# Performance work log

Hardware: AMD Instinct MI355X
Metric: run time of the kernel (lower is better)

The kernel has to match this reference:

```python
import jax, jax.numpy as jnp
import numpy as np

B, S, D = 8, 2048, 512
E, DF = 16, 2048  # total experts, FFN hidden (4*d_model)
K = 4             # num_available_experts


def setup_inputs() -> dict:
    key = jax.random.key(0)
    ks = jax.random.split(key, 5)
    scale = 0.02
    return {
        "x": jax.random.normal(ks[0], (B, S, D), dtype=jnp.float32),
        "gate_w": jax.random.normal(ks[1], (E, D), dtype=jnp.float32) * scale,
        "gate_b": jnp.zeros((E,), dtype=jnp.float32),
        "w1": jax.random.normal(ks[2], (E, D, DF), dtype=jnp.float32) * scale,
        "b1": jnp.zeros((E, DF), dtype=jnp.float32),
        "w2": jax.random.normal(ks[3], (E, DF, D), dtype=jnp.float32) * scale,
        "b2": jnp.zeros((E, D), dtype=jnp.float32),
        "num_available": K,
    }


def reference(x, gate_w, gate_b, w1, b1, w2, b2, num_available):
    # Coarse expert selection: gate applied to the global token sum k = sum_{b,s} x
    k = jnp.sum(x, axis=(0, 1))                       # [D]
    coarse = gate_w @ k + gate_b                      # [E]
    _, idx = jax.lax.top_k(coarse, num_available)     # [K]

    # Gather selected experts' params
    gw_w, gw_b = gate_w[idx], gate_b[idx]             # [K,D], [K]
    W1, B1 = w1[idx], b1[idx]                         # [K,D,DF], [K,DF]
    W2, B2 = w2[idx], b2[idx]                         # [K,DF,D], [K,D]

    # Per-token softmax gating over the K selected experts
    logits = jnp.einsum('bsd,kd->bsk', x, gw_w) + gw_b  # [B,S,K]
    gw = jax.nn.softmax(logits, axis=2)                 # [B,S,K]

    # Dense expert FFNs over all tokens, weighted combine
    h = jax.nn.gelu(jnp.einsum('bsd,kdf->kbsf', x, W1) + B1[:, None, None, :])  # [K,B,S,DF]
    eo = jnp.einsum('kbsf,kfd->kbsd', h, W2) + B2[:, None, None, :]             # [K,B,S,D]
    out = jnp.einsum('kbsd,bsk->bsd', eo, gw)                                   # [B,S,D]
    return out
```

## Files before the change

### kernel.cpp

```cpp
#include <hip/hip_runtime.h>
#include <hip/hip_bf16.h>
#include <cstdint>
#include <cstddef>

typedef __attribute__((ext_vector_type(8))) short short8;
typedef __attribute__((ext_vector_type(4))) float f32x4;

#define AS1U32(p) ((const __attribute__((address_space(1))) uint32_t*)(p))
#define AS3U32(p) ((__attribute__((address_space(3))) uint32_t*)(p))

__device__ __forceinline__ unsigned short f2bf(float v) {
  union { float f; uint32_t u; } a; a.f = v;
  uint32_t u = a.u;
  u += 0x7FFFu + ((u >> 16) & 1u);
  return (unsigned short)(u >> 16);
}

__device__ __forceinline__ float gelu_fast(float x) {
  const float A = -2.302118142f;
  const float B = -0.102943494f;
  float x2 = x * x;
  float t = x * __builtin_fmaf(B, x2, A);
  float e = __builtin_amdgcn_exp2f(t);
  return x * __builtin_amdgcn_rcpf(1.0f + e);
}


__global__ __launch_bounds__(512)
void reduce_part(const float* __restrict__ x, float* __restrict__ kpart) {
  const int d = threadIdx.x;
  const int b = blockIdx.x;
  float s = 0.f;
#pragma unroll 4
  for (int i = 0; i < 64; i++)
    s += x[((size_t)b * 64 + i) * 512 + d];
  kpart[(size_t)b * 512 + d] = s;
}

__global__ __launch_bounds__(1024)
void gate_all(const float* __restrict__ kpart,
              const float* __restrict__ gate_w,
              const float* __restrict__ gate_b,
              const float* __restrict__ b1, const float* __restrict__ b2,
              int* __restrict__ idxout,
              float* __restrict__ b1cat, float* __restrict__ b2sel) {
  __shared__ float ksum2[2][512];
  __shared__ float coarse[16];
  __shared__ int idxl[4];
  const int t = threadIdx.x;
  {
    const int d = t & 511, h = t >> 9;
    float s = 0.f;
    for (int p = h * 128; p < h * 128 + 128; p++) s += kpart[(size_t)p * 512 + d];
    ksum2[h][d] = s;
  }
  __syncthreads();
  {
    const int wave = t >> 6, lane = t & 63;
    const int d0 = lane * 8;
    float s = 0.f;
#pragma unroll
    for (int j = 0; j < 8; j++)
      s += gate_w[wave * 512 + d0 + j] * (ksum2[0][d0 + j] + ksum2[1][d0 + j]);
#pragma unroll
    for (int off = 32; off >= 1; off >>= 1) s += __shfl_down(s, off, 64);
    if (lane == 0) coarse[wave] = s + gate_b[wave];
  }
  __syncthreads();
  if (t == 0) {
    unsigned taken = 0;
    for (int r = 0; r < 4; r++) {
      float best = -3.4e38f; int bi = 0;
      for (int e = 0; e < 16; e++)
        if (!((taken >> e) & 1u) && coarse[e] > best) { best = coarse[e]; bi = e; }
      taken |= 1u << bi;
      idxl[r] = bi; idxout[r] = bi;
    }
  }
  __syncthreads();
  for (int i = t; i < 8192; i += 1024)
    b1cat[i] = b1[(size_t)idxl[i >> 11] * 2048 + (i & 2047)];
  for (int i = t; i < 2048; i += 1024)
    b2sel[i] = b2[(size_t)idxl[i >> 9] * 512 + (i & 511)];
}

__global__ __launch_bounds__(256)
void transpose_all(const float* __restrict__ w1, const float* __restrict__ w2,
                   unsigned short* __restrict__ w1t, unsigned short* __restrict__ w2t,
                   const int* __restrict__ idx) {
  __shared__ float tl[64][65];
  const int tid = threadIdx.x;
  const int ty = tid >> 6, tx = tid & 63;
  const int z = blockIdx.z;
  const float* src; unsigned short* dbase; int C, dstLd, r0, c0;
  if (z < 4) {
    src = w1 + (size_t)idx[z] * 512 * 2048;
    dbase = w1t + (size_t)z * 2048 * 512;
    C = 2048; dstLd = 512;
    r0 = blockIdx.x * 64; c0 = blockIdx.y * 64;
  } else {
    src = w2 + (size_t)idx[z - 4] * 2048 * 512;
    dbase = w2t + (size_t)(z - 4) * 2048;
    C = 512; dstLd = 8192;
    r0 = blockIdx.y * 64; c0 = blockIdx.x * 64;
  }
#pragma unroll
  for (int i = 0; i < 16; i++) {
    int r = ty * 16 + i;
    tl[r][tx] = src[(size_t)(r0 + r) * C + c0 + tx];
  }
  __syncthreads();
#pragma unroll
  for (int i = 0; i < 16; i++) {
    int rr = ty * 16 + i;
    dbase[(size_t)(c0 + rr) * dstLd + r0 + tx] = f2bf(tl[tx][rr]);
  }
}

__global__ __launch_bounds__(256)
void gate_softmax_xconv(const float* __restrict__ x,
                        const float* __restrict__ gate_w,
                        const float* __restrict__ gate_b,
                        const int* __restrict__ idx,
                        float* __restrict__ gwout,
                        unsigned short* __restrict__ xbf) {
  __shared__ float wsel[4][512];
  __shared__ float bsel[4];
  const int tid = threadIdx.x;
  for (int i = tid; i < 2048; i += 256) {
    int k = i >> 9;
    wsel[k][i & 511] = gate_w[(size_t)idx[k] * 512 + (i & 511)];
  }
  if (tid < 4) bsel[tid] = gate_b[idx[tid]];
  __syncthreads();
  const int wave = tid >> 6, lane = tid & 63;
  const int t = blockIdx.x * 4 + wave;
  const float* xr = x + (size_t)t * 512 + lane * 8;
  float4 v0 = ((const float4*)xr)[0];
  float4 v1 = ((const float4*)xr)[1];
  float vals[8] = {v0.x, v0.y, v0.z, v0.w, v1.x, v1.y, v1.z, v1.w};
  short8 pk;
#pragma unroll
  for (int j = 0; j < 8; j++) pk[j] = (short)f2bf(vals[j]);
  *(short8*)(xbf + (size_t)t * 512 + lane * 8) = pk;
  float a0 = 0.f, a1 = 0.f, a2 = 0.f, a3 = 0.f;
  const int dbase = lane * 8;
#pragma unroll
  for (int j = 0; j < 8; j++) {
    float xv = vals[j];
    a0 += xv * wsel[0][dbase + j];
    a1 += xv * wsel[1][dbase + j];
    a2 += xv * wsel[2][dbase + j];
    a3 += xv * wsel[3][dbase + j];
  }
#pragma unroll
  for (int off = 32; off >= 1; off >>= 1) {
    a0 += __shfl_down(a0, off, 64);
    a1 += __shfl_down(a1, off, 64);
    a2 += __shfl_down(a2, off, 64);
    a3 += __shfl_down(a3, off, 64);
  }
  if (lane == 0) {
    float l0 = a0 + bsel[0], l1 = a1 + bsel[1], l2 = a2 + bsel[2], l3 = a3 + bsel[3];
    float m = fmaxf(fmaxf(l0, l1), fmaxf(l2, l3));
    float e0 = __expf(l0 - m), e1 = __expf(l1 - m);
    float e2 = __expf(l2 - m), e3 = __expf(l3 - m);
    float inv = 1.0f / (e0 + e1 + e2 + e3);
    float* o = gwout + (size_t)t * 4;
    o[0] = e0 * inv; o[1] = e1 * inv; o[2] = e2 * inv; o[3] = e3 * inv;
  }
}


#define CFENCE asm volatile("" ::: "memory")
#define BAR    do { CFENCE; __builtin_amdgcn_s_barrier(); CFENCE; } while (0)
#define LGKM0  do { asm volatile("s_waitcnt lgkmcnt(0)" ::: "memory"); \
                    __builtin_amdgcn_sched_barrier(0); } while (0)
#define SCHEDB __builtin_amdgcn_sched_barrier(0)
#define VMW(n) asm volatile("s_waitcnt vmcnt(" #n ")" ::: "memory")

#define LDALL(abuf, bbuf)                                                   \
  do {                                                                      \
    _Pragma("unroll")                                                       \
    for (int i_ = 0; i_ < 4; i_++)                                          \
      _Pragma("unroll")                                                     \
      for (int ks_ = 0; ks_ < 2; ks_++)                                     \
        aF[i_][ks_] = *(const short8*)((abuf) +                             \
            (size_t)(wm + i_ * 16 + fr) * 64 +                              \
            (((ks_ * 4 + quad) ^ swz) << 3));                               \
    _Pragma("unroll")                                                       \
    for (int j_ = 0; j_ < 4; j_++)                                          \
      _Pragma("unroll")                                                     \
      for (int ks_ = 0; ks_ < 2; ks_++)                                     \
        bF[j_][ks_] = *(const short8*)((bbuf) +                             \
            (size_t)(wn + j_ * 16 + fr) * 64 +                              \
            (((ks_ * 4 + quad) ^ swz) << 3));                               \
  } while (0)

#define MMH(ks)                                                             \
  do {                                                                      \
    __builtin_amdgcn_s_setprio(1);                                          \
    _Pragma("unroll")                                                       \
    for (int i_ = 0; i_ < 4; i_++)                                          \
      _Pragma("unroll")                                                     \
      for (int j_ = 0; j_ < 4; j_++)                                        \
        acc[i_][j_] = __builtin_amdgcn_mfma_f32_16x16x32_bf16(              \
            aF[i_][ks], bF[j_][ks], acc[i_][j_], 0, 0, 0);                  \
    __builtin_amdgcn_s_setprio(0);                                          \
  } while (0)

template <int EPI>
__global__ __launch_bounds__(256, 2)
void gemm4p(const unsigned short* __restrict__ A,
            const unsigned short* __restrict__ Bt,
            void* __restrict__ C, int K, int lda, int ldb, int ldc,
            const float* __restrict__ gw,
            const float* __restrict__ bias, int colOff, int accum) {
  __shared__ unsigned short lds[4 * 128 * 64];
  const int tid = threadIdx.x;
  const int wave = tid >> 6, lane = tid & 63;
  const int lrow = lane >> 3, lslot = lane & 7, gch = lslot ^ lrow;
  const int fr = lane & 15, quad = lane >> 4, swz = fr & 7;
  const int wm = (wave >> 1) * 64, wn = (wave & 1) * 64;
  const int rowA0 = blockIdx.x * 128;
  const int rowB0 = blockIdx.y * 128;

  unsigned short* const A0 = lds;
  unsigned short* const B0 = lds + 128 * 64;
  unsigned short* const A1 = lds + 2 * 128 * 64;
  unsigned short* const B1 = lds + 3 * 128 * 64;

  auto stT = [&](unsigned short* ab, unsigned short* bb, int kt) {
#pragma unroll
    for (int c = 0; c < 4; c++) {
      int r = wave * 32 + c * 8 + lrow;
      const unsigned short* gp = A + (size_t)(rowA0 + r) * lda + kt + gch * 8;
      __builtin_amdgcn_global_load_lds(AS1U32(gp), AS3U32(ab + (wave * 32 + c * 8) * 64), 16, 0, 0);
    }
#pragma unroll
    for (int c = 0; c < 4; c++) {
      int r = wave * 32 + c * 8 + lrow;
      const unsigned short* gp = Bt + (size_t)(rowB0 + r) * ldb + kt + gch * 8;
      __builtin_amdgcn_global_load_lds(AS1U32(gp), AS3U32(bb + (wave * 32 + c * 8) * 64), 16, 0, 0);
    }
  };

  f32x4 acc[4][4];
#pragma unroll
  for (int i = 0; i < 4; i++)
#pragma unroll
    for (int j = 0; j < 4; j++) acc[i][j] = (f32x4){0.f, 0.f, 0.f, 0.f};

  short8 aF[4][2];
  short8 bF[4][2];

  stT(A0, B0, 0);
  stT(A1, B1, 64);
  VMW(8);
  BAR;

  const int niter = K >> 7;
  for (int i = 0; i < niter - 1; i++) {
    const int kt = i * 128;
    LDALL(A0, B0);
    BAR; LGKM0; MMH(0); BAR;
    stT(A0, B0, kt + 128); SCHEDB;
    MMH(1); VMW(8); BAR;
    LDALL(A1, B1);
    BAR; LGKM0; MMH(0); BAR;
    stT(A1, B1, kt + 192); SCHEDB;
    MMH(1); VMW(8); BAR;
  }
  LDALL(A0, B0);
  BAR; LGKM0; MMH(0); BAR;
  MMH(1); VMW(0); BAR;
  LDALL(A1, B1);
  BAR; LGKM0; MMH(0); BAR;
  MMH(1);

  if (EPI == 1) {
    unsigned short* Cb = (unsigned short*)C;
    const int kexp = (colOff + rowB0) >> 11;
#pragma unroll
    for (int i = 0; i < 4; i++) {
#pragma unroll
      for (int reg = 0; reg < 4; reg++) {
        int r = rowA0 + wm + i * 16 + quad * 4 + reg;
        float g = gw[(size_t)r * 4 + kexp];
#pragma unroll
        for (int j = 0; j < 4; j++) {
          int n = rowB0 + wn + j * 16 + fr;
          float v = acc[i][j][reg] + bias[colOff + n];
          Cb[(size_t)r * ldc + n] = f2bf(gelu_fast(v) * g);
        }
      }
    }
  } else {
    float* Cf = (float*)C;
#pragma unroll
    for (int i = 0; i < 4; i++) {
#pragma unroll
      for (int reg = 0; reg < 4; reg++) {
        int r = rowA0 + wm + i * 16 + quad * 4 + reg;
        size_t t4 = (size_t)r * 4;
        float g0 = gw[t4], g1 = gw[t4 + 1], g2 = gw[t4 + 2], g3 = gw[t4 + 3];
#pragma unroll
        for (int j = 0; j < 4; j++) {
          int n = rowB0 + wn + j * 16 + fr;
          size_t ci = (size_t)r * 512 + n;
          float v = acc[i][j][reg];
          if (accum) v += Cf[ci];
          else v += g0 * bias[n] + g1 * bias[512 + n] +
                    g2 * bias[1024 + n] + g3 * bias[1536 + n];
          Cf[ci] = v;
        }
      }
    }
  }
}

#undef LDALL
#undef MMH


extern "C" void kernel_launch(void* const* d_in, const int* in_sizes, int n_in,
                              void* d_out, int out_size, void* d_ws, size_t ws_size,
                              hipStream_t stream) {
  (void)in_sizes; (void)n_in; (void)out_size;
  const float* x      = (const float*)d_in[0];
  const float* gate_w = (const float*)d_in[1];
  const float* gate_b = (const float*)d_in[2];
  const float* w1     = (const float*)d_in[3];
  const float* b1     = (const float*)d_in[4];
  const float* w2     = (const float*)d_in[5];
  const float* b2     = (const float*)d_in[6];

  char* ws = (char*)d_ws;
  int*            idx   = (int*)(ws + 0);
  float*          gw    = (float*)(ws + 4096);
  float*          b1cat = (float*)(ws + 266240);
  float*          b2sel = (float*)(ws + 299008);
  float*          kpart = (float*)(ws + 307200);
  unsigned short* xbf   = (unsigned short*)(ws + 831488);
  unsigned short* w1t   = (unsigned short*)(ws + 17608704);
  unsigned short* w2t   = (unsigned short*)(ws + 25997312);
  unsigned short* hbuf  = (unsigned short*)(ws + 34385920);
  const size_t HBUF_OFF = 34385920;

  size_t avail = ws_size > HBUF_OFF ? ws_size - HBUF_OFF : 0;
  int nslab = 1;
  while (nslab < 16 && (size_t)16384 * (8192 / nslab) * 2 > avail) nslab <<= 1;
  const int slabDF = 8192 / nslab;

  reduce_part<<<256, 512, 0, stream>>>(x, kpart);
  gate_all<<<1, 1024, 0, stream>>>(kpart, gate_w, gate_b, b1, b2, idx, b1cat, b2sel);
  transpose_all<<<dim3(8, 32, 8), 256, 0, stream>>>(w1, w2, w1t, w2t, idx);
  gate_softmax_xconv<<<4096, 256, 0, stream>>>(x, gate_w, gate_b, idx, gw, xbf);

  for (int s = 0; s < nslab; s++) {
    const int c0 = s * slabDF;
    gemm4p<1><<<dim3(128, slabDF / 128), 256, 0, stream>>>(
        xbf, w1t + (size_t)c0 * 512, hbuf,
        512, 512, 512, slabDF,
        gw, b1cat, c0, 0);
    gemm4p<2><<<dim3(128, 4), 256, 0, stream>>>(
        hbuf, w2t + c0, (float*)d_out,
        slabDF, slabDF, 8192, 512,
        gw, b2sel, 0, s > 0);
  }
}
```

Before: 502.1 us.

## Fuse prep kernels, vectorize transpose, and add simpler direct-to-LDS GEMM for first FFN

Merges the weight transpose and the gate-softmax/bf16-conversion kernels into one launch. The transpose now moves float4/ushort4 vectors per thread. The first FFN GEMM is replaced by a new single-buffered GEMM that loads global memory straight into swizzled LDS and runs bf16 MFMA 16x16x32 with two blocks per CU. The token-sum reduction also uses fewer, longer partial sums. This cuts launch overhead and narrow memory accesses, but the new GEMM drops the software pipelining of the old gemm4p and may hide memory latency less well.

```diff
diff --git a/kernel.cpp b/kernel.cpp
--- a/kernel.cpp
+++ b/kernel.cpp
@@ -32,8 +32,8 @@
   const int b = blockIdx.x;
   float s = 0.f;
 #pragma unroll 4
-  for (int i = 0; i < 64; i++)
-    s += x[((size_t)b * 64 + i) * 512 + d];
+  for (int i = 0; i < 128; i++)
+    s += x[((size_t)b * 128 + i) * 512 + d];
   kpart[(size_t)b * 512 + d] = s;
 }
 
@@ -51,7 +51,7 @@
   {
     const int d = t & 511, h = t >> 9;
     float s = 0.f;
-    for (int p = h * 128; p < h * 128 + 128; p++) s += kpart[(size_t)p * 512 + d];
+    for (int p = h * 64; p < h * 64 + 64; p++) s += kpart[(size_t)p * 512 + d];
     ksum2[h][d] = s;
   }
   __syncthreads();
@@ -85,89 +85,206 @@
 }
 
 __global__ __launch_bounds__(256)
-void transpose_all(const float* __restrict__ w1, const float* __restrict__ w2,
-                   unsigned short* __restrict__ w1t, unsigned short* __restrict__ w2t,
-                   const int* __restrict__ idx) {
-  __shared__ float tl[64][65];
+void prep_fused(const float* __restrict__ x,
+                const float* __restrict__ gate_w,
+                const float* __restrict__ gate_b,
+                const int* __restrict__ idx,
+                float* __restrict__ gwout,
+                unsigned short* __restrict__ xbf,
+                const float* __restrict__ w1, const float* __restrict__ w2,
+                unsigned short* __restrict__ w1t, unsigned short* __restrict__ w2t) {
+  __shared__ float smem[64 * 65];
   const int tid = threadIdx.x;
-  const int ty = tid >> 6, tx = tid & 63;
-  const int z = blockIdx.z;
-  const float* src; unsigned short* dbase; int C, dstLd, r0, c0;
-  if (z < 4) {
-    src = w1 + (size_t)idx[z] * 512 * 2048;
-    dbase = w1t + (size_t)z * 2048 * 512;
-    C = 2048; dstLd = 512;
-    r0 = blockIdx.x * 64; c0 = blockIdx.y * 64;
+  const int bid = blockIdx.x;
+
+  if (bid < 4096) {
+    float* wsel = smem;
+    float* bsel = smem + 2048;
+    for (int i = tid; i < 2048; i += 256) {
+      int k = i >> 9;
+      wsel[(size_t)k * 512 + (i & 511)] = gate_w[(size_t)idx[k] * 512 + (i & 511)];
+    }
+    if (tid < 4) bsel[tid] = gate_b[idx[tid]];
+    __syncthreads();
+    const int wave = tid >> 6, lane = tid & 63;
+    const int t = bid * 4 + wave;
+    const float* xr = x + (size_t)t * 512 + lane * 8;
+    float4 v0 = ((const float4*)xr)[0];
+    float4 v1 = ((const float4*)xr)[1];
+    float vals[8] = {v0.x, v0.y, v0.z, v0.w, v1.x, v1.y, v1.z, v1.w};
+    short8 pk;
+#pragma unroll
+    for (int j = 0; j < 8; j++) pk[j] = (short)f2bf(vals[j]);
+    *(short8*)(xbf + (size_t)t * 512 + lane * 8) = pk;
+    float a0 = 0.f, a1 = 0.f, a2 = 0.f, a3 = 0.f;
+    const int dbase = lane * 8;
+#pragma unroll
+    for (int j = 0; j < 8; j++) {
+      float xv = vals[j];
+      a0 += xv * wsel[dbase + j];
+      a1 += xv * wsel[512 + dbase + j];
+      a2 += xv * wsel[1024 + dbase + j];
+      a3 += xv * wsel[1536 + dbase + j];
+    }
+#pragma unroll
+    for (int off = 32; off >= 1; off >>= 1) {
+      a0 += __shfl_down(a0, off, 64);
+      a1 += __shfl_down(a1, off, 64);
+      a2 += __shfl_down(a2, off, 64);
+      a3 += __shfl_down(a3, off, 64);
+    }
+    if (lane == 0) {
+      float l0 = a0 + bsel[0], l1 = a1 + bsel[1], l2 = a2 + bsel[2], l3 = a3 + bsel[3];
+      float m = fmaxf(fmaxf(l0, l1), fmaxf(l2, l3));
+      float e0 = __expf(l0 - m), e1 = __expf(l1 - m);
+      float e2 = __expf(l2 - m), e3 = __expf(l3 - m);
+      float inv = 1.0f / (e0 + e1 + e2 + e3);
+      float* o = gwout + (size_t)t * 4;
+      o[0] = e0 * inv; o[1] = e1 * inv; o[2] = e2 * inv; o[3] = e3 * inv;
+    }
   } else {
-    src = w2 + (size_t)idx[z - 4] * 2048 * 512;
-    dbase = w2t + (size_t)(z - 4) * 2048;
-    C = 512; dstLd = 8192;
-    r0 = blockIdx.y * 64; c0 = blockIdx.x * 64;
-  }
-#pragma unroll
-  for (int i = 0; i < 16; i++) {
-    int r = ty * 16 + i;
-    tl[r][tx] = src[(size_t)(r0 + r) * C + c0 + tx];
-  }
-  __syncthreads();
-#pragma unroll
-  for (int i = 0; i < 16; i++) {
-    int rr = ty * 16 + i;
-    dbase[(size_t)(c0 + rr) * dstLd + r0 + tx] = f2bf(tl[tx][rr]);
-  }
-}
-
-__global__ __launch_bounds__(256)
-void gate_softmax_xconv(const float* __restrict__ x,
-                        const float* __restrict__ gate_w,
-                        const float* __restrict__ gate_b,
-                        const int* __restrict__ idx,
-                        float* __restrict__ gwout,
-                        unsigned short* __restrict__ xbf) {
-  __shared__ float wsel[4][512];
-  __shared__ float bsel[4];
+    const int zz = bid - 4096;
+    const int z = zz >> 8;
+    const int rem = zz & 255;
+    const int bx = rem & 7, by = rem >> 3;
+    const float* src; unsigned short* dbase; int C, dstLd, r0, c0;
+    if (z < 4) {
+      src = w1 + (size_t)idx[z] * 512 * 2048;
+      dbase = w1t + (size_t)z * 2048 * 512;
+      C = 2048; dstLd = 512;
+      r0 = bx * 64; c0 = by * 64;
+    } else {
+      src = w2 + (size_t)idx[z - 4] * 2048 * 512;
+      dbase = w2t + (size_t)(z - 4) * 2048;
+      C = 512; dstLd = 8192;
+      r0 = by * 64; c0 = bx * 64;
+    }
+    float (*tl)[65] = (float(*)[65])smem;
+    const int tx4 = (tid & 15) * 4;
+    const int ty = tid >> 4;
+#pragma unroll
+    for (int i = 0; i < 4; i++) {
+      int r = i * 16 + ty;
+      float4 v = *(const float4*)&src[(size_t)(r0 + r) * C + c0 + tx4];
+      tl[r][tx4 + 0] = v.x; tl[r][tx4 + 1] = v.y;
+      tl[r][tx4 + 2] = v.z; tl[r][tx4 + 3] = v.w;
+    }
+    __syncthreads();
+#pragma unroll
+    for (int i = 0; i < 4; i++) {
+      int rr = i * 16 + ty;
+      ushort4 o;
+      o.x = f2bf(tl[tx4 + 0][rr]);
+      o.y = f2bf(tl[tx4 + 1][rr]);
+      o.z = f2bf(tl[tx4 + 2][rr]);
+      o.w = f2bf(tl[tx4 + 3][rr]);
+      *(ushort4*)&dbase[(size_t)(c0 + rr) * dstLd + r0 + tx4] = o;
+    }
+  }
+}
+
+template <int EPI>
+__global__ __launch_bounds__(256, 2)
+void gemm_bt(const unsigned short* __restrict__ A,
+             const unsigned short* __restrict__ Bt,
+             void* __restrict__ C, int K, int lda, int ldb, int ldc,
+             const float* __restrict__ gw,
+             const float* __restrict__ bias, int colOff, int accum) {
+  __shared__ unsigned short lA[128 * 64];
+  __shared__ unsigned short lB[128 * 64];
   const int tid = threadIdx.x;
-  for (int i = tid; i < 2048; i += 256) {
-    int k = i >> 9;
-    wsel[k][i & 511] = gate_w[(size_t)idx[k] * 512 + (i & 511)];
-  }
-  if (tid < 4) bsel[tid] = gate_b[idx[tid]];
-  __syncthreads();
-  const int wave = tid >> 6, lane = tid & 63;
-  const int t = blockIdx.x * 4 + wave;
-  const float* xr = x + (size_t)t * 512 + lane * 8;
-  float4 v0 = ((const float4*)xr)[0];
-  float4 v1 = ((const float4*)xr)[1];
-  float vals[8] = {v0.x, v0.y, v0.z, v0.w, v1.x, v1.y, v1.z, v1.w};
-  short8 pk;
-#pragma unroll
-  for (int j = 0; j < 8; j++) pk[j] = (short)f2bf(vals[j]);
-  *(short8*)(xbf + (size_t)t * 512 + lane * 8) = pk;
-  float a0 = 0.f, a1 = 0.f, a2 = 0.f, a3 = 0.f;
-  const int dbase = lane * 8;
-#pragma unroll
-  for (int j = 0; j < 8; j++) {
-    float xv = vals[j];
-    a0 += xv * wsel[0][dbase + j];
-    a1 += xv * wsel[1][dbase + j];
-    a2 += xv * wsel[2][dbase + j];
-    a3 += xv * wsel[3][dbase + j];
-  }
-#pragma unroll
-  for (int off = 32; off >= 1; off >>= 1) {
-    a0 += __shfl_down(a0, off, 64);
-    a1 += __shfl_down(a1, off, 64);
-    a2 += __shfl_down(a2, off, 64);
-    a3 += __shfl_down(a3, off, 64);
-  }
-  if (lane == 0) {
-    float l0 = a0 + bsel[0], l1 = a1 + bsel[1], l2 = a2 + bsel[2], l3 = a3 + bsel[3];
-    float m = fmaxf(fmaxf(l0, l1), fmaxf(l2, l3));
-    float e0 = __expf(l0 - m), e1 = __expf(l1 - m);
-    float e2 = __expf(l2 - m), e3 = __expf(l3 - m);
-    float inv = 1.0f / (e0 + e1 + e2 + e3);
-    float* o = gwout + (size_t)t * 4;
-    o[0] = e0 * inv; o[1] = e1 * inv; o[2] = e2 * inv; o[3] = e3 * inv;
+  const int wave = tid >> 6;
+  const int lane = tid & 63;
+  const int rowA0 = blockIdx.x * 128;
+  const int rowB0 = blockIdx.y * 128;
+
+  f32x4 acc[4][4];
+#pragma unroll
+  for (int i = 0; i < 4; i++)
+#pragma unroll
+    for (int j = 0; j < 4; j++) acc[i][j] = (f32x4){0.f, 0.f, 0.f, 0.f};
+
+  const int lrow = lane >> 3;
+  const int lslot = lane & 7;
+  const int gchunk = lslot ^ lrow;
+  const int fr = lane & 15;
+  const int quad = lane >> 4;
+  const int wm = (wave >> 1) * 64;
+  const int wn = (wave & 1) * 64;
+  const int swz = fr & 7;
+
+  for (int kt = 0; kt < K; kt += 64) {
+#pragma unroll
+    for (int c = 0; c < 4; c++) {
+      int r = wave * 32 + c * 8 + lrow;
+      const unsigned short* gp = A + (size_t)(rowA0 + r) * lda + kt + gchunk * 8;
+      __builtin_amdgcn_global_load_lds(AS1U32(gp), AS3U32(lA + (wave * 32 + c * 8) * 64), 16, 0, 0);
+    }
+#pragma unroll
+    for (int c = 0; c < 4; c++) {
+      int r = wave * 32 + c * 8 + lrow;
+      const unsigned short* gp = Bt + (size_t)(rowB0 + r) * ldb + kt + gchunk * 8;
+      __builtin_amdgcn_global_load_lds(AS1U32(gp), AS3U32(lB + (wave * 32 + c * 8) * 64), 16, 0, 0);
+    }
+    __syncthreads();
+#pragma unroll
+    for (int ks = 0; ks < 2; ks++) {
+      short8 af[4], bfr[4];
+      const int c = ks * 4 + quad;
+      const int slot = (c ^ swz) << 3;
+#pragma unroll
+      for (int i = 0; i < 4; i++)
+        af[i] = *(const short8*)(lA + (wm + i * 16 + fr) * 64 + slot);
+#pragma unroll
+      for (int j = 0; j < 4; j++)
+        bfr[j] = *(const short8*)(lB + (wn + j * 16 + fr) * 64 + slot);
+#pragma unroll
+      for (int i = 0; i < 4; i++)
+#pragma unroll
+        for (int j = 0; j < 4; j++)
+          acc[i][j] = __builtin_amdgcn_mfma_f32_16x16x32_bf16(af[i], bfr[j], acc[i][j], 0, 0, 0);
+    }
+    __syncthreads();
+  }
+
+  if (EPI == 1) {
+    unsigned short* Cb = (unsigned short*)C;
+    const int kexp = (colOff + rowB0) >> 11;
+#pragma unroll
+    for (int i = 0; i < 4; i++) {
+#pragma unroll
+      for (int reg = 0; reg < 4; reg++) {
+        int r = rowA0 + wm + i * 16 + quad * 4 + reg;
+        float g = gw[(size_t)r * 4 + kexp];
+#pragma unroll
+        for (int j = 0; j < 4; j++) {
+          int n = rowB0 + wn + j * 16 + fr;
+          float v = acc[i][j][reg] + bias[colOff + n];
+          Cb[(size_t)r * ldc + n] = f2bf(gelu_fast(v) * g);
+        }
+      }
+    }
+  } else {
+    float* Cf = (float*)C;
+#pragma unroll
+    for (int i = 0; i < 4; i++) {
+#pragma unroll
+      for (int reg = 0; reg < 4; reg++) {
+        int r = rowA0 + wm + i * 16 + quad * 4 + reg;
+        size_t t4 = (size_t)r * 4;
+        float g0 = gw[t4], g1 = gw[t4 + 1], g2 = gw[t4 + 2], g3 = gw[t4 + 3];
+#pragma unroll
+        for (int j = 0; j < 4; j++) {
+          int n = rowB0 + wn + j * 16 + fr;
+          size_t ci = (size_t)r * 512 + n;
+          float v = acc[i][j][reg];
+          if (accum) v += Cf[ci];
+          else v += g0 * bias[n] + g1 * bias[512 + n] +
+                    g2 * bias[1024 + n] + g3 * bias[1536 + n];
+          Cf[ci] = v;
+        }
+      }
+    }
   }
 }
 
@@ -352,14 +469,14 @@
   while (nslab < 16 && (size_t)16384 * (8192 / nslab) * 2 > avail) nslab <<= 1;
   const int slabDF = 8192 / nslab;
 
-  reduce_part<<<256, 512, 0, stream>>>(x, kpart);
+  reduce_part<<<128, 512, 0, stream>>>(x, kpart);
   gate_all<<<1, 1024, 0, stream>>>(kpart, gate_w, gate_b, b1, b2, idx, b1cat, b2sel);
-  transpose_all<<<dim3(8, 32, 8), 256, 0, stream>>>(w1, w2, w1t, w2t, idx);
-  gate_softmax_xconv<<<4096, 256, 0, stream>>>(x, gate_w, gate_b, idx, gw, xbf);
+  prep_fused<<<6144, 256, 0, stream>>>(x, gate_w, gate_b, idx, gw, xbf,
+                                       w1, w2, w1t, w2t);
 
   for (int s = 0; s < nslab; s++) {
     const int c0 = s * slabDF;
-    gemm4p<1><<<dim3(128, slabDF / 128), 256, 0, stream>>>(
+    gemm_bt<1><<<dim3(128, slabDF / 128), 256, 0, stream>>>(
         xbf, w1t + (size_t)c0 * 512, hbuf,
         512, 512, 512, slabDF,
         gw, b1cat, c0, 0);
```

New measurement: 515.2 us. 2.6% more time.
